# Performance work log

Hardware: AMD Instinct MI355X
Metric: run time of the kernel (lower is better)

## Reference

```python
import jax, jax.numpy as jnp
import numpy as np

N = 8192
IN_DIM = 128
HID = 32


def setup_inputs() -> dict:
    key = jax.random.key(0)
    ks = jax.random.split(key, 8)
    x = jax.random.normal(ks[0], (N, IN_DIM), dtype=jnp.float32)
    adj = jax.random.uniform(ks[1], (N, N), dtype=jnp.float32)
    # Linear params (torch nn.Linear: y = x @ W.T + b); store as [in, out] for einsum.
    def lin(k, fan_in, fan_out):
        bound = 1.0 / np.sqrt(fan_in)
        kw, kb = jax.random.split(k)
        W = jax.random.uniform(kw, (fan_in, fan_out), minval=-bound, maxval=bound, dtype=jnp.float32)
        b = jax.random.uniform(kb, (fan_out,), minval=-bound, maxval=bound, dtype=jnp.float32)
        return W, b
    W1, b1 = lin(ks[2], IN_DIM, HID)
    W2, b2 = lin(ks[3], HID, HID)
    W3, b3 = lin(ks[4], HID, 1)
    return {"x": x, "adj": adj, "W1": W1, "b1": b1, "W2": W2, "b2": b2, "W3": W3, "b3": b3}


def reference(x, adj, W1, b1, W2, b2, W3, b3):
    # a_hat = adj + I (self loops)
    n = adj.shape[0]
    a_hat = adj + jnp.eye(n, dtype=adj.dtype)
    degree = jnp.sum(a_hat, axis=1)
    d_inv_sqrt = jnp.clip(degree, 1.0, None) ** -0.5  # [N]
    # D^-1/2 A D^-1/2 as row/col scaling (same math as diag matmuls, no O(N^3) waste)
    a_norm = d_inv_sqrt[:, None] * a_hat * d_inv_sqrt[None, :]
    h = jax.nn.relu(a_norm @ (x @ W1 + b1))
    h = jax.nn.relu(a_norm @ (h @ W2 + b2))
    logits = (h @ W3 + b3).squeeze(-1)  # [N]
    return logits
```

## Files before the change

kernel.cpp:

```cpp
#include <hip/hip_runtime.h>
#include <math.h>

#define N 8192
#define IN_DIM 128
#define HID 32

#define RB 128
#define KT 64
#define SK 8
#define KCHUNK (N / SK)

__device__ __forceinline__ void fma4(float4& acc, float a, const float4& b) {
    acc.x = fmaf(a, b.x, acc.x);
    acc.y = fmaf(a, b.y, acc.y);
    acc.z = fmaf(a, b.z, acc.z);
    acc.w = fmaf(a, b.w, acc.w);
}

__global__ __launch_bounds__(256) void k_degree(const float* __restrict__ adj,
                                                float* __restrict__ dinv) {
    int row = blockIdx.x;
    const float4* rp = (const float4*)(adj + (size_t)row * N);
    int t = threadIdx.x;
    float s = 0.f;
#pragma unroll
    for (int i = 0; i < 8; ++i) {
        float4 v = rp[t + i * 256];
        s += v.x + v.y + v.z + v.w;
    }
    for (int off = 32; off > 0; off >>= 1) s += __shfl_down(s, off, 64);
    __shared__ float red[4];
    if ((t & 63) == 0) red[t >> 6] = s;
    __syncthreads();
    if (t == 0) {
        float deg = red[0] + red[1] + red[2] + red[3] + 1.0f;
        deg = fmaxf(deg, 1.0f);
        dinv[row] = 1.0f / sqrtf(deg);
    }
}

__global__ __launch_bounds__(256) void k_z1(const float* __restrict__ x,
                                            const float* __restrict__ W1,
                                            const float* __restrict__ b1,
                                            const float* __restrict__ dinv,
                                            float* __restrict__ Zs) {
    __shared__ float Ws[IN_DIM * HID];
    __shared__ float xs[8 * IN_DIM];
    int t = threadIdx.x;
    int row0 = blockIdx.x * 8;
#pragma unroll
    for (int i = 0; i < 4; ++i)
        *(float4*)&Ws[(i * 256 + t) * 4] = *(const float4*)&W1[(i * 256 + t) * 4];
    *(float4*)&xs[t * 4] = *(const float4*)&x[(size_t)row0 * IN_DIM + t * 4];
    __syncthreads();
    int r = t >> 5, c = t & 31;
    float acc = b1[c];
#pragma unroll 8
    for (int k = 0; k < IN_DIM; ++k) acc = fmaf(xs[r * IN_DIM + k], Ws[k * HID + c], acc);
    int row = row0 + r;
    Zs[(size_t)row * HID + c] = dinv[row] * acc;
}

__global__ __launch_bounds__(256) void k_z2(const float* __restrict__ Hin,
                                            const float* __restrict__ W2,
                                            const float* __restrict__ b2,
                                            const float* __restrict__ dinv,
                                            float* __restrict__ Zs) {
    __shared__ float Ws[HID * HID];
    __shared__ float hs[8 * HID];
    int t = threadIdx.x;
    int row0 = blockIdx.x * 8;
    *(float4*)&Ws[t * 4] = *(const float4*)&W2[t * 4];
    if (t < 64) *(float4*)&hs[t * 4] = *(const float4*)&Hin[(size_t)row0 * HID + t * 4];
    __syncthreads();
    int r = t >> 5, c = t & 31;
    float acc = b2[c];
#pragma unroll
    for (int k = 0; k < HID; ++k) acc = fmaf(hs[r * HID + k], Ws[k * HID + c], acc);
    int row = row0 + r;
    Zs[(size_t)row * HID + c] = dinv[row] * acc;
}

__global__ __launch_bounds__(256) void k_spmm(const float* __restrict__ adj,
                                              const float* __restrict__ Zs,
                                              float* __restrict__ P) {
    __shared__ float As[RB][KT + 4];
    __shared__ float Bs[KT][HID];
    int t = threadIdx.x;
    int r0 = blockIdx.x * RB;
    int k0 = blockIdx.y * KCHUNK;
    int cg = t & 3;
    int rp2 = (t >> 2) * 2;
    float4 acc00 = {0, 0, 0, 0}, acc01 = {0, 0, 0, 0};
    float4 acc10 = {0, 0, 0, 0}, acc11 = {0, 0, 0, 0};

    for (int kt = k0; kt < k0 + KCHUNK; kt += KT) {
#pragma unroll
        for (int i = 0; i < 8; ++i) {
            int f = i * 256 + t;
            int row = f >> 4;
            int kc = (f & 15) << 2;
            *(float4*)&As[row][kc] = *(const float4*)&adj[(size_t)(r0 + row) * N + kt + kc];
        }
#pragma unroll
        for (int i = 0; i < 2; ++i) {
            int f = i * 256 + t;
            ((float4*)&Bs[0][0])[f] = ((const float4*)(Zs + (size_t)kt * HID))[f];
        }
        __syncthreads();
#pragma unroll
        for (int kk = 0; kk < KT; kk += 4) {
            float a0[4], a1[4];
            *(float4*)a0 = *(const float4*)&As[rp2][kk];
            *(float4*)a1 = *(const float4*)&As[rp2 + 1][kk];
#pragma unroll
            for (int j = 0; j < 4; ++j) {
                float4 z0 = *(const float4*)&Bs[kk + j][cg * 8];
                float4 z1 = *(const float4*)&Bs[kk + j][cg * 8 + 4];
                fma4(acc00, a0[j], z0);
                fma4(acc01, a0[j], z1);
                fma4(acc10, a1[j], z0);
                fma4(acc11, a1[j], z1);
            }
        }
        __syncthreads();
    }

    float* p0 = P + (size_t)(r0 + rp2) * HID + cg * 8;
    float* p1 = p0 + HID;
    atomicAdd(p0 + 0, acc00.x); atomicAdd(p0 + 1, acc00.y);
    atomicAdd(p0 + 2, acc00.z); atomicAdd(p0 + 3, acc00.w);
    atomicAdd(p0 + 4, acc01.x); atomicAdd(p0 + 5, acc01.y);
    atomicAdd(p0 + 6, acc01.z); atomicAdd(p0 + 7, acc01.w);
    atomicAdd(p1 + 0, acc10.x); atomicAdd(p1 + 1, acc10.y);
    atomicAdd(p1 + 2, acc10.z); atomicAdd(p1 + 3, acc10.w);
    atomicAdd(p1 + 4, acc11.x); atomicAdd(p1 + 5, acc11.y);
    atomicAdd(p1 + 6, acc11.z); atomicAdd(p1 + 7, acc11.w);
}

__global__ __launch_bounds__(256) void k_fin(const float* __restrict__ P,
                                             const float* __restrict__ Zs,
                                             const float* __restrict__ dinv,
                                             float* __restrict__ H) {
    int idx = blockIdx.x * 256 + threadIdx.x;
    int row = idx >> 5;
    float v = dinv[row] * (P[idx] + Zs[idx]);
    H[idx] = fmaxf(v, 0.f);
}

__global__ __launch_bounds__(256) void k_out(const float* __restrict__ H,
                                             const float* __restrict__ W3,
                                             const float* __restrict__ b3,
                                             float* __restrict__ out) {
    int i = blockIdx.x * 256 + threadIdx.x;
    const float4* hr = (const float4*)(H + (size_t)i * HID);
    const float4* w = (const float4*)W3;
    float acc = b3[0];
#pragma unroll
    for (int kk = 0; kk < 8; ++kk) {
        float4 h = hr[kk], ww = w[kk];
        acc += h.x * ww.x + h.y * ww.y + h.z * ww.z + h.w * ww.w;
    }
    out[i] = acc;
}

extern "C" void kernel_launch(void* const* d_in, const int* in_sizes, int n_in,
                              void* d_out, int out_size, void* d_ws, size_t ws_size,
                              hipStream_t stream) {
    const float* x   = (const float*)d_in[0];
    const float* adj = (const float*)d_in[1];
    const float* W1  = (const float*)d_in[2];
    const float* b1  = (const float*)d_in[3];
    const float* W2  = (const float*)d_in[4];
    const float* b2  = (const float*)d_in[5];
    const float* W3  = (const float*)d_in[6];
    const float* b3  = (const float*)d_in[7];
    float* out = (float*)d_out;

    float* dinv = (float*)d_ws;
    float* Zs   = dinv + N;
    float* P    = Zs + (size_t)N * HID;
    float* H    = P + (size_t)N * HID;

    k_degree<<<N, 256, 0, stream>>>(adj, dinv);
    k_z1<<<N / 8, 256, 0, stream>>>(x, W1, b1, dinv, Zs);

    hipMemsetAsync(P, 0, (size_t)N * HID * sizeof(float), stream);
    k_spmm<<<dim3(N / RB, SK), 256, 0, stream>>>(adj, Zs, P);
    k_fin<<<N * HID / 256, 256, 0, stream>>>(P, Zs, dinv, H);

    k_z2<<<N / 8, 256, 0, stream>>>(H, W2, b2, dinv, Zs);

    hipMemsetAsync(P, 0, (size_t)N * HID * sizeof(float), stream);
    k_spmm<<<dim3(N / RB, SK), 256, 0, stream>>>(adj, Zs, P);
    k_fin<<<N * HID / 256, 256, 0, stream>>>(P, Zs, dinv, H);

    k_out<<<N / 256, 256, 0, stream>>>(H, W3, b3, out);
}
```

Baseline: 612.7 us.

## Replace atomic split-K with partial buffers, swizzle LDS, fuse finalize kernels

```diff
diff --git a/kernel.cpp b/kernel.cpp
--- a/kernel.cpp
+++ b/kernel.cpp
@@ -7,7 +7,7 @@
 
 #define RB 128
 #define KT 64
-#define SK 8
+#define SK 16
 #define KCHUNK (N / SK)
 
 __device__ __forceinline__ void fma4(float4& acc, float a, const float4& b) {
@@ -61,36 +61,17 @@
     Zs[(size_t)row * HID + c] = dinv[row] * acc;
 }
 
-__global__ __launch_bounds__(256) void k_z2(const float* __restrict__ Hin,
-                                            const float* __restrict__ W2,
-                                            const float* __restrict__ b2,
-                                            const float* __restrict__ dinv,
-                                            float* __restrict__ Zs) {
-    __shared__ float Ws[HID * HID];
-    __shared__ float hs[8 * HID];
-    int t = threadIdx.x;
-    int row0 = blockIdx.x * 8;
-    *(float4*)&Ws[t * 4] = *(const float4*)&W2[t * 4];
-    if (t < 64) *(float4*)&hs[t * 4] = *(const float4*)&Hin[(size_t)row0 * HID + t * 4];
-    __syncthreads();
-    int r = t >> 5, c = t & 31;
-    float acc = b2[c];
-#pragma unroll
-    for (int k = 0; k < HID; ++k) acc = fmaf(hs[r * HID + k], Ws[k * HID + c], acc);
-    int row = row0 + r;
-    Zs[(size_t)row * HID + c] = dinv[row] * acc;
-}
-
 __global__ __launch_bounds__(256) void k_spmm(const float* __restrict__ adj,
                                               const float* __restrict__ Zs,
                                               float* __restrict__ P) {
-    __shared__ float As[RB][KT + 4];
+    __shared__ float As[RB * KT];
     __shared__ float Bs[KT][HID];
     int t = threadIdx.x;
     int r0 = blockIdx.x * RB;
     int k0 = blockIdx.y * KCHUNK;
     int cg = t & 3;
     int rp2 = (t >> 2) * 2;
+    int e = (rp2 >> 1) & 7;
     float4 acc00 = {0, 0, 0, 0}, acc01 = {0, 0, 0, 0};
     float4 acc10 = {0, 0, 0, 0}, acc11 = {0, 0, 0, 0};
 
@@ -99,8 +80,10 @@
         for (int i = 0; i < 8; ++i) {
             int f = i * 256 + t;
             int row = f >> 4;
-            int kc = (f & 15) << 2;
-            *(float4*)&As[row][kc] = *(const float4*)&adj[(size_t)(r0 + row) * N + kt + kc];
+            int fi = f & 15;
+            int sfi = fi ^ ((row >> 1) & 7);
+            *(float4*)&As[row * KT + sfi * 4] =
+                *(const float4*)&adj[(size_t)(r0 + row) * N + kt + fi * 4];
         }
 #pragma unroll
         for (int i = 0; i < 2; ++i) {
@@ -110,9 +93,10 @@
         __syncthreads();
 #pragma unroll
         for (int kk = 0; kk < KT; kk += 4) {
+            int s0 = ((kk >> 2) ^ e) * 4;
             float a0[4], a1[4];
-            *(float4*)a0 = *(const float4*)&As[rp2][kk];
-            *(float4*)a1 = *(const float4*)&As[rp2 + 1][kk];
+            *(float4*)a0 = *(const float4*)&As[rp2 * KT + s0];
+            *(float4*)a1 = *(const float4*)&As[(rp2 + 1) * KT + s0];
 #pragma unroll
             for (int j = 0; j < 4; ++j) {
                 float4 z0 = *(const float4*)&Bs[kk + j][cg * 8];
@@ -126,42 +110,57 @@
         __syncthreads();
     }
 
-    float* p0 = P + (size_t)(r0 + rp2) * HID + cg * 8;
+    float* p0 = P + (size_t)blockIdx.y * (N * HID) + (size_t)(r0 + rp2) * HID + cg * 8;
     float* p1 = p0 + HID;
-    atomicAdd(p0 + 0, acc00.x); atomicAdd(p0 + 1, acc00.y);
-    atomicAdd(p0 + 2, acc00.z); atomicAdd(p0 + 3, acc00.w);
-    atomicAdd(p0 + 4, acc01.x); atomicAdd(p0 + 5, acc01.y);
-    atomicAdd(p0 + 6, acc01.z); atomicAdd(p0 + 7, acc01.w);
-    atomicAdd(p1 + 0, acc10.x); atomicAdd(p1 + 1, acc10.y);
-    atomicAdd(p1 + 2, acc10.z); atomicAdd(p1 + 3, acc10.w);
-    atomicAdd(p1 + 4, acc11.x); atomicAdd(p1 + 5, acc11.y);
-    atomicAdd(p1 + 6, acc11.z); atomicAdd(p1 + 7, acc11.w);
+    *(float4*)(p0)     = acc00;
+    *(float4*)(p0 + 4) = acc01;
+    *(float4*)(p1)     = acc10;
+    *(float4*)(p1 + 4) = acc11;
 }
 
-__global__ __launch_bounds__(256) void k_fin(const float* __restrict__ P,
-                                             const float* __restrict__ Zs,
-                                             const float* __restrict__ dinv,
-                                             float* __restrict__ H) {
-    int idx = blockIdx.x * 256 + threadIdx.x;
-    int row = idx >> 5;
-    float v = dinv[row] * (P[idx] + Zs[idx]);
-    H[idx] = fmaxf(v, 0.f);
+__global__ __launch_bounds__(256) void k_fin_z2(const float* __restrict__ P,
+                                                const float* __restrict__ Zin,
+                                                const float* __restrict__ dinv,
+                                                const float* __restrict__ W2,
+                                                const float* __restrict__ b2,
+                                                float* __restrict__ Zout) {
+    __shared__ float Ws[HID * HID];
+    __shared__ float hs[8][HID];
+    int t = threadIdx.x;
+    int row0 = blockIdx.x * 8;
+    *(float4*)&Ws[t * 4] = *(const float4*)&W2[t * 4];
+    int r = t >> 5, c = t & 31;
+    size_t idx = (size_t)row0 * HID + t;
+    float v = Zin[idx];
+#pragma unroll
+    for (int s = 0; s < SK; ++s) v += P[(size_t)s * (N * HID) + idx];
+    int row = row0 + r;
+    hs[r][c] = fmaxf(dinv[row] * v, 0.f);
+    __syncthreads();
+    float acc = b2[c];
+#pragma unroll
+    for (int k = 0; k < HID; ++k) acc = fmaf(hs[r][k], Ws[k * HID + c], acc);
+    Zout[idx] = dinv[row] * acc;
 }
 
-__global__ __launch_bounds__(256) void k_out(const float* __restrict__ H,
-                                             const float* __restrict__ W3,
-                                             const float* __restrict__ b3,
-                                             float* __restrict__ out) {
-    int i = blockIdx.x * 256 + threadIdx.x;
-    const float4* hr = (const float4*)(H + (size_t)i * HID);
-    const float4* w = (const float4*)W3;
-    float acc = b3[0];
+__global__ __launch_bounds__(256) void k_fin_out(const float* __restrict__ P,
+                                                 const float* __restrict__ Zin,
+                                                 const float* __restrict__ dinv,
+                                                 const float* __restrict__ W3,
+                                                 const float* __restrict__ b3,
+                                                 float* __restrict__ out) {
+    int t = threadIdx.x;
+    size_t idx = (size_t)blockIdx.x * 256 + t;
+    int row = (int)(idx >> 5);
+    int c = t & 31;
+    float v = Zin[idx];
 #pragma unroll
-    for (int kk = 0; kk < 8; ++kk) {
-        float4 h = hr[kk], ww = w[kk];
-        acc += h.x * ww.x + h.y * ww.y + h.z * ww.z + h.w * ww.w;
-    }
-    out[i] = acc;
+    for (int s = 0; s < SK; ++s) v += P[(size_t)s * (N * HID) + idx];
+    float h = fmaxf(dinv[row] * v, 0.f);
+    float hw = h * W3[c];
+#pragma unroll
+    for (int off = 16; off > 0; off >>= 1) hw += __shfl_xor(hw, off, 32);
+    if (c == 0) out[row] = hw + b3[0];
 }
 
 extern "C" void kernel_launch(void* const* d_in, const int* in_sizes, int n_in,
@@ -178,22 +177,16 @@
     float* out = (float*)d_out;
 
     float* dinv = (float*)d_ws;
-    float* Zs   = dinv + N;
-    float* P    = Zs + (size_t)N * HID;
-    float* H    = P + (size_t)N * HID;
+    float* Zs1  = dinv + N;
+    float* Zs2  = Zs1 + (size_t)N * HID;
+    float* P    = Zs2 + (size_t)N * HID;
 
     k_degree<<<N, 256, 0, stream>>>(adj, dinv);
-    k_z1<<<N / 8, 256, 0, stream>>>(x, W1, b1, dinv, Zs);
+    k_z1<<<N / 8, 256, 0, stream>>>(x, W1, b1, dinv, Zs1);
 
-    hipMemsetAsync(P, 0, (size_t)N * HID * sizeof(float), stream);
-    k_spmm<<<dim3(N / RB, SK), 256, 0, stream>>>(adj, Zs, P);
-    k_fin<<<N * HID / 256, 256, 0, stream>>>(P, Zs, dinv, H);
+    k_spmm<<<dim3(N / RB, SK), 256, 0, stream>>>(adj, Zs1, P);
+    k_fin_z2<<<N / 8, 256, 0, stream>>>(P, Zs1, dinv, W2, b2, Zs2);
 
-    k_z2<<<N / 8, 256, 0, stream>>>(H, W2, b2, dinv, Zs);
-
-    hipMemsetAsync(P, 0, (size_t)N * HID * sizeof(float), stream);
-    k_spmm<<<dim3(N / RB, SK), 256, 0, stream>>>(adj, Zs, P);
-    k_fin<<<N * HID / 256, 256, 0, stream>>>(P, Zs, dinv, H);
-
-    k_out<<<N / 256, 256, 0, stream>>>(H, W3, b3, out);
+    k_spmm<<<dim3(N / RB, SK), 256, 0, stream>>>(adj, Zs2, P);
+    k_fin_out<<<N * HID / 256, 256, 0, stream>>>(P, Zs2, dinv, W3, b3, out);
 }
```

New measurement: 522.8 us. 14.7% less time.
